# Optimization experiments

Hardware: AMD Instinct MI355X
Metric: run time of the kernel (lower is better)

## Reference

```python
import jax, jax.numpy as jnp
import jax.lax as lax
import numpy as np

PS = 5           # patch_w for rgb (arch_opt.rgb=True)
PAD = PS // 2    # 2
WS = 29          # search window
SRAD = WS // 2   # 14
K = 14           # neigh_pad: number of nearest neighbors kept


def setup_inputs() -> dict:
    key = jax.random.key(0)
    k1, k2 = jax.random.split(key)
    noisy = jax.random.uniform(k1, (1, 3, 256, 256), jnp.float32) * 255.0
    sigma = jnp.array([25.0], jnp.float32)
    w_gray = jnp.array([0.2989, 0.587, 0.114], jnp.float32)  # fixed rgb2gray conv weight
    return {"noisy": noisy, "sigma": sigma, "w_gray": w_gray}


def reference(noisy, sigma, w_gray):
    t, c, h, w = noisy.shape
    # rescale to [-1,1] and remove per-image mean (as in forward)
    x = (noisy / 255.0 - 0.5) / 0.5
    means = x.mean((-2, -1), keepdims=True)
    x = x - means

    # grayscale search image (rgb2gray 1x1 conv)
    g = jnp.einsum('tchw,c->thw', x, w_gray)
    padT = PAD + SRAD  # 16: patch halo + search radius
    Gp = jnp.pad(g, ((0, 0), (padT, padT), (padT, padT)), mode='reflect')

    # --- patch-SSD over all ws*ws window offsets (KNN search) ---
    offs = jnp.arange(WS * WS)
    dys, dxs = offs // WS, offs % WS  # 0..28 <-> true offset -14..14
    Hc, Wc = h + 2 * PAD, w + 2 * PAD

    def crop(dy, dx):  # shifted crop covering all query patch supports
        return lax.dynamic_slice(Gp, (0, dy, dx), (t, Hc, Wc))

    S = jax.vmap(crop)(dys, dxs)                                   # [O,t,Hc,Wc]
    Cc = lax.dynamic_slice(Gp, (0, SRAD, SRAD), (t, Hc, Wc))       # center crop
    diff2 = (Cc[None] - S) ** 2                                    # [O,t,Hc,Wc]
    O = WS * WS
    kern = jnp.ones((1, 1, PS, PS), jnp.float32)
    d = lax.conv_general_dilated(diff2.reshape(O * t, 1, Hc, Wc), kern,
                                 (1, 1), 'VALID',
                                 dimension_numbers=('NCHW', 'OIHW', 'NCHW'))
    dists = d.reshape(O, t, h, w).transpose(1, 2, 3, 0)            # [t,h,w,O]

    negd, idx = lax.top_k(-dists, K)                               # k nearest offsets
    dists_k = -negd                                                # [t,h,w,K]

    # --- gather neighbor color patches ---
    Xp = jnp.pad(x, ((0, 0), (0, 0), (padT, padT), (padT, padT)), mode='reflect')
    patches = lax.conv_general_dilated_patches(Xp, (PS, PS), (1, 1), 'VALID')
    D = c * PS * PS
    Hg, Wg = h + 2 * SRAD, w + 2 * SRAD   # patch-center grid incl. search halo
    pf = patches.reshape(t, D, Hg * Wg)
    dy, dx = idx // WS, idx % WS          # 0..28; grid row = i + dy
    ii = jnp.arange(h)[None, :, None, None]
    jj = jnp.arange(w)[None, None, :, None]
    flat = ((ii + dy) * Wg + (jj + dx)).reshape(t, -1)             # [t, h*w*K]
    gathered = jax.vmap(lambda p, f: jnp.take(p, f, axis=1))(pf, flat)
    gathered = gathered.reshape(t, D, h * w, K)                    # [t,D,Q,K]

    # --- distance-softmax weighted patch aggregation ---
    sig = sigma[0] / 127.5  # noise std in rescaled units
    wts = jax.nn.softmax(-dists_k.reshape(t, h * w, K) / (sig * sig * PS * PS + 1e-8), axis=-1)
    pden = jnp.einsum('tdqk,tqk->tdq', gathered, wts).reshape(t, c, PS, PS, h, w)

    # --- fold (overlap-add) denoised patches + count normalization ---
    out = jnp.zeros((t, c, Hc, Wc), jnp.float32)
    cnt = jnp.zeros((1, 1, Hc, Wc), jnp.float32)
    for p in range(PS):
        for q in range(PS):
            out = out.at[:, :, p:p + h, q:q + w].add(pden[:, :, p, q])
            cnt = cnt.at[:, :, p:p + h, q:q + w].add(1.0)
    deno = out[:, :, PAD:-PAD, PAD:-PAD] / cnt[:, :, PAD:-PAD, PAD:-PAD]

    deno = deno + means
    deno = 255.0 * (deno * 0.5 + 0.5)
    return deno
```

## Files before the change

### kernel.cpp

```cpp
#include <hip/hip_runtime.h>

#define EXT 40
#define SQ (EXT*EXT)

__device__ __forceinline__ unsigned um_min(unsigned a, unsigned b){ return a < b ? a : b; }
__device__ __forceinline__ unsigned um_max(unsigned a, unsigned b){ return a > b ? a : b; }

__device__ __forceinline__ void insert14(unsigned (&arr)[14], unsigned key){
  arr[0] = um_min(arr[0], key);
  #pragma unroll
  for (int s = 0; s < 13; ++s){
    unsigned a = arr[s], b = arr[s+1];
    arr[s]   = um_max(a, b);
    arr[s+1] = um_min(a, b);
  }
}

__global__ void k_prep(const float* __restrict__ noisy, float* __restrict__ Xp){
  int idx = blockIdx.x * 256 + threadIdx.x;
  if (idx >= 288*288) return;
  int P = idx / 288, Q = idx - P*288;
  int sy = P - 16; sy = sy < 0 ? -sy : sy; sy = sy > 255 ? 510 - sy : sy;
  int sx = Q - 16; sx = sx < 0 ? -sx : sx; sx = sx > 255 ? 510 - sx : sx;
  const float inv = 1.0f / 127.5f;
  int src = sy*256 + sx;
  #pragma unroll
  for (int c = 0; c < 3; ++c)
    Xp[c*82944 + idx] = noisy[c*65536 + src] * inv - 1.0f;
}

template<int R>
__device__ __forceinline__ void ssd_step(const float* rowbase, int dx, unsigned obase,
                                         float (&cp)[5][5], float (&win)[5][5],
                                         unsigned (&arr)[14]){
  constexpr int nc = (R + 4) % 5;
  #pragma unroll
  for (int u = 0; u < 5; ++u) win[u][nc] = rowbase[u*EXT + dx + 4];
  float s = 0.f;
  #pragma unroll
  for (int u = 0; u < 5; ++u){
    #pragma unroll
    for (int v = 0; v < 5; ++v){
      float d = cp[u][v] - win[u][(R + v) % 5];
      s = fmaf(d, d, s);
    }
  }
  insert14(arr, (__float_as_uint(s) & 0xFFFFFC00u) | (obase + (unsigned)dx));
}

__global__ __launch_bounds__(256, 4) void k_search(const float* __restrict__ Xp,
      const float* __restrict__ sigma, const float* __restrict__ wgray,
      float* __restrict__ accG){
  __shared__ float sXp[3*SQ];
  __shared__ float sG[SQ];
  __shared__ unsigned sCand[3*64*14];
  __shared__ float sWsum[64];
  __shared__ float sFold[12*12*3];

  const int tid = threadIdx.x;
  const int w = tid >> 6, l = tid & 63;
  const int ly = l >> 3, lx = l & 7;
  const int bi = blockIdx.y * 8, bj = blockIdx.x * 8;

  for (int t = tid; t < 3*SQ; t += 256){
    int c = t / SQ; int r2 = t - c*SQ; int rr = r2 / EXT; int cc = r2 - rr*EXT;
    sXp[t] = Xp[c*82944 + (bi+rr)*288 + (bj+cc)];
  }
  if (tid < 64) sWsum[tid] = 0.f;
  for (int t = tid; t < 432; t += 256) sFold[t] = 0.f;
  __syncthreads();
  const float w0 = wgray[0], w1 = wgray[1], w2 = wgray[2];
  for (int t = tid; t < SQ; t += 256)
    sG[t] = w0*sXp[t] + w1*sXp[SQ+t] + w2*sXp[2*SQ+t];
  __syncthreads();

  float cp[5][5];
  #pragma unroll
  for (int u = 0; u < 5; ++u)
    #pragma unroll
    for (int v = 0; v < 5; ++v)
      cp[u][v] = sG[(14 + ly + u)*EXT + 14 + lx + v];

  unsigned arr[14];
  #pragma unroll
  for (int k = 0; k < 14; ++k) arr[k] = 0xFFFFFFFFu;

  const int dy0 = (w == 0) ? 0 : 1 + 7*w;
  const int dy1 = dy0 + ((w == 0) ? 8 : 7);

  for (int dy = dy0; dy < dy1; ++dy){
    const float* rowbase = &sG[(dy + ly)*EXT + lx];
    float win[5][5];
    #pragma unroll
    for (int u = 0; u < 5; ++u)
      #pragma unroll
      for (int v = 0; v < 4; ++v)
        win[u][v] = rowbase[u*EXT + v];
    const unsigned obase = (unsigned)(dy * 29);

    for (int b = 0; b < 5; ++b){
      int dxb = b * 5;
      ssd_step<0>(rowbase, dxb+0, obase, cp, win, arr);
      ssd_step<1>(rowbase, dxb+1, obase, cp, win, arr);
      ssd_step<2>(rowbase, dxb+2, obase, cp, win, arr);
      ssd_step<3>(rowbase, dxb+3, obase, cp, win, arr);
      ssd_step<4>(rowbase, dxb+4, obase, cp, win, arr);
    }
    ssd_step<0>(rowbase, 25, obase, cp, win, arr);
    ssd_step<1>(rowbase, 26, obase, cp, win, arr);
    ssd_step<2>(rowbase, 27, obase, cp, win, arr);
    ssd_step<3>(rowbase, 28, obase, cp, win, arr);
  }

  if (w){
    #pragma unroll
    for (int k = 0; k < 14; ++k) sCand[((w-1)*64 + l)*14 + k] = arr[k];
  }
  __syncthreads();
  if (!w){
    for (int q = 0; q < 3; ++q)
      #pragma unroll
      for (int k = 0; k < 14; ++k)
        insert14(arr, sCand[(q*64 + l)*14 + k]);
    #pragma unroll
    for (int k = 0; k < 14; ++k) sCand[l*14 + k] = arr[k];
  }
  __syncthreads();

  float sg = sigma[0] * (1.0f / 127.5f);
  const float invT = 1.0f / (sg*sg*25.0f + 1e-8f);
  const float dmin = __uint_as_float(sCand[l*14 + 13] & 0xFFFFFC00u);

  float wgt[4]; int ndy[4], ndx[4];
  const int nk = (w < 2) ? 4 : 3;
  float Sp = 0.f;
  #pragma unroll
  for (int m = 0; m < 4; ++m){
    if (m < nk){
      unsigned kk = sCand[l*14 + (w + 4*m)];
      float d = __uint_as_float(kk & 0xFFFFFC00u);
      int o = (int)(kk & 0x3FFu);
      wgt[m] = expf(-(d - dmin) * invT);
      ndy[m] = o / 29; ndx[m] = o - ndy[m]*29;
      Sp += wgt[m];
    }
  }
  atomicAdd(&sWsum[l], Sp);
  __syncthreads();
  const float invS = 1.0f / sWsum[l];
  #pragma unroll
  for (int m = 0; m < 4; ++m) if (m < nk) wgt[m] *= invS;

  #pragma unroll
  for (int c = 0; c < 3; ++c){
    float acc[5][5];
    #pragma unroll
    for (int u = 0; u < 5; ++u)
      #pragma unroll
      for (int v = 0; v < 5; ++v) acc[u][v] = 0.f;
    #pragma unroll
    for (int m = 0; m < 4; ++m){
      if (m < nk){
        const float* pb = &sXp[c*SQ + (ly + ndy[m])*EXT + lx + ndx[m]];
        float g = wgt[m];
        #pragma unroll
        for (int u = 0; u < 5; ++u)
          #pragma unroll
          for (int v = 0; v < 5; ++v)
            acc[u][v] = fmaf(g, pb[u*EXT + v], acc[u][v]);
      }
    }
    #pragma unroll
    for (int u = 0; u < 5; ++u)
      #pragma unroll
      for (int v = 0; v < 5; ++v)
        atomicAdd(&sFold[((ly+u)*12 + (lx+v))*3 + c], acc[u][v]);
  }
  __syncthreads();
  for (int t = tid; t < 432; t += 256){
    int c = t % 3; int rc = t / 3; int rr = rc / 12; int cc = rc - rr*12;
    atomicAdd(&accG[c*67600 + (bi+rr)*260 + (bj+cc)], sFold[t]);
  }
}

__global__ void k_finish(const float* __restrict__ accG, float* __restrict__ out){
  int idx = blockIdx.x * 256 + threadIdx.x;
  if (idx >= 3*65536) return;
  int c = idx >> 16; int rem = idx & 65535; int y = rem >> 8; int x = rem & 255;
  int cy = min(4, y + 2) - max(0, y - 253) + 1;
  int cx = min(4, x + 2) - max(0, x - 253) + 1;
  float v = accG[c*67600 + (y+2)*260 + (x+2)] / (float)(cy * cx);
  out[idx] = 127.5f * v + 127.5f;
}

extern "C" void kernel_launch(void* const* d_in, const int* in_sizes, int n_in,
                              void* d_out, int out_size, void* d_ws, size_t ws_size,
                              hipStream_t stream) {
  const float* noisy = (const float*)d_in[0];
  const float* sigma = (const float*)d_in[1];
  const float* wgray = (const float*)d_in[2];
  float* out  = (float*)d_out;
  float* Xp   = (float*)d_ws;
  float* accG = Xp + 3*288*288;

  hipMemsetAsync(accG, 0, 3*260*260*sizeof(float), stream);
  k_prep<<<dim3(324), dim3(256), 0, stream>>>(noisy, Xp);
  k_search<<<dim3(32, 32), dim3(256), 0, stream>>>(Xp, sigma, wgray, accG);
  k_finish<<<dim3(768), dim3(256), 0, stream>>>(accG, out);
}
```

Before: 254.9 us.

## Expand SSD into norms minus cross term, use med3 top-k insert, fuse memset

```diff
diff --git a/kernel.cpp b/kernel.cpp
--- a/kernel.cpp
+++ b/kernel.cpp
@@ -5,19 +5,29 @@
 
 __device__ __forceinline__ unsigned um_min(unsigned a, unsigned b){ return a < b ? a : b; }
 __device__ __forceinline__ unsigned um_max(unsigned a, unsigned b){ return a > b ? a : b; }
-
-__device__ __forceinline__ void insert14(unsigned (&arr)[14], unsigned key){
-  arr[0] = um_min(arr[0], key);
-  #pragma unroll
-  for (int s = 0; s < 13; ++s){
-    unsigned a = arr[s], b = arr[s+1];
-    arr[s]   = um_max(a, b);
-    arr[s+1] = um_min(a, b);
-  }
-}
-
-__global__ void k_prep(const float* __restrict__ noisy, float* __restrict__ Xp){
+__device__ __forceinline__ unsigned med3u(unsigned a, unsigned b, unsigned c){
+  unsigned d;
+  asm("v_med3_u32 %0, %1, %2, %3" : "=v"(d) : "v"(a), "v"(b), "v"(c));
+  return d;
+}
+
+__device__ __forceinline__ void insert14(unsigned (&a)[14], unsigned key){
+  unsigned kp  = um_min(key, a[0]);
+  unsigned n0  = um_max(a[1], kp);
+  unsigned n13 = um_min(a[13], kp);
+  unsigned nn[12];
+  #pragma unroll
+  for (int i = 1; i <= 12; ++i) nn[i-1] = med3u(a[i], a[i+1], kp);
+  a[0] = n0;
+  #pragma unroll
+  for (int i = 1; i <= 12; ++i) a[i] = nn[i-1];
+  a[13] = n13;
+}
+
+__global__ void k_prep(const float* __restrict__ noisy, float* __restrict__ Xp,
+                       float* __restrict__ accG){
   int idx = blockIdx.x * 256 + threadIdx.x;
+  if (idx < 3*260*260) accG[idx] = 0.f;
   if (idx >= 288*288) return;
   int P = idx / 288, Q = idx - P*288;
   int sy = P - 16; sy = sy < 0 ? -sy : sy; sy = sy > 255 ? 510 - sy : sy;
@@ -29,23 +39,44 @@
     Xp[c*82944 + idx] = noisy[c*65536 + src] * inv - 1.0f;
 }
 
-template<int R>
-__device__ __forceinline__ void ssd_step(const float* rowbase, int dx, unsigned obase,
-                                         float (&cp)[5][5], float (&win)[5][5],
-                                         unsigned (&arr)[14]){
-  constexpr int nc = (R + 4) % 5;
-  #pragma unroll
-  for (int u = 0; u < 5; ++u) win[u][nc] = rowbase[u*EXT + dx + 4];
-  float s = 0.f;
-  #pragma unroll
-  for (int u = 0; u < 5; ++u){
-    #pragma unroll
-    for (int v = 0; v < 5; ++v){
-      float d = cp[u][v] - win[u][(R + v) % 5];
-      s = fmaf(d, d, s);
-    }
-  }
-  insert14(arr, (__float_as_uint(s) & 0xFFFFFC00u) | (obase + (unsigned)dx));
+template<int DX>
+__device__ __forceinline__ void ssd_step(const float* rowbase, unsigned obase,
+                                         const float (&cp)[5][5], float cpsq,
+                                         float (&win)[5][5], float (&ring)[5],
+                                         float& winsq, unsigned (&arr)[14]){
+  constexpr int nc = (DX + 4) % 5;
+  #pragma unroll
+  for (int u = 0; u < 5; ++u) win[u][nc] = rowbase[u*EXT + DX + 4];
+  float nssq = win[0][nc]*win[0][nc];
+  #pragma unroll
+  for (int u = 1; u < 5; ++u) nssq = fmaf(win[u][nc], win[u][nc], nssq);
+  winsq += (nssq - ring[nc]);
+  ring[nc] = nssq;
+  float c0=0.f, c1=0.f, c2=0.f, c3=0.f, c4=0.f;
+  #pragma unroll
+  for (int v = 0; v < 5; ++v){
+    constexpr int dummy = 0; (void)dummy;
+    c0 = fmaf(cp[0][v], win[0][(DX + v) % 5], c0);
+    c1 = fmaf(cp[1][v], win[1][(DX + v) % 5], c1);
+    c2 = fmaf(cp[2][v], win[2][(DX + v) % 5], c2);
+    c3 = fmaf(cp[3][v], win[3][(DX + v) % 5], c3);
+    c4 = fmaf(cp[4][v], win[4][(DX + v) % 5], c4);
+  }
+  float cross = ((c0 + c1) + (c2 + c3)) + c4;
+  float dist = fmaf(cross, -2.0f, cpsq + winsq);
+  dist = fmaxf(dist, 0.0f);
+  insert14(arr, (__float_as_uint(dist) & 0xFFFFFC00u) | (obase + (unsigned)DX));
+}
+
+template<int DX>
+__device__ __forceinline__ void row_steps(const float* rowbase, unsigned obase,
+                                          const float (&cp)[5][5], float cpsq,
+                                          float (&win)[5][5], float (&ring)[5],
+                                          float& winsq, unsigned (&arr)[14]){
+  if constexpr (DX < 29){
+    ssd_step<DX>(rowbase, obase, cp, cpsq, win, ring, winsq, arr);
+    row_steps<DX+1>(rowbase, obase, cp, cpsq, win, ring, winsq, arr);
+  }
 }
 
 __global__ __launch_bounds__(256, 4) void k_search(const float* __restrict__ Xp,
@@ -80,6 +111,14 @@
     #pragma unroll
     for (int v = 0; v < 5; ++v)
       cp[u][v] = sG[(14 + ly + u)*EXT + 14 + lx + v];
+  float cpsq = 0.f;
+  #pragma unroll
+  for (int v = 0; v < 5; ++v){
+    float cs = cp[0][v]*cp[0][v];
+    #pragma unroll
+    for (int u = 1; u < 5; ++u) cs = fmaf(cp[u][v], cp[u][v], cs);
+    cpsq += cs;
+  }
 
   unsigned arr[14];
   #pragma unroll
@@ -88,28 +127,22 @@
   const int dy0 = (w == 0) ? 0 : 1 + 7*w;
   const int dy1 = dy0 + ((w == 0) ? 8 : 7);
 
+  #pragma unroll 1
   for (int dy = dy0; dy < dy1; ++dy){
     const float* rowbase = &sG[(dy + ly)*EXT + lx];
-    float win[5][5];
-    #pragma unroll
-    for (int u = 0; u < 5; ++u)
-      #pragma unroll
-      for (int v = 0; v < 4; ++v)
-        win[u][v] = rowbase[u*EXT + v];
-    const unsigned obase = (unsigned)(dy * 29);
-
-    for (int b = 0; b < 5; ++b){
-      int dxb = b * 5;
-      ssd_step<0>(rowbase, dxb+0, obase, cp, win, arr);
-      ssd_step<1>(rowbase, dxb+1, obase, cp, win, arr);
-      ssd_step<2>(rowbase, dxb+2, obase, cp, win, arr);
-      ssd_step<3>(rowbase, dxb+3, obase, cp, win, arr);
-      ssd_step<4>(rowbase, dxb+4, obase, cp, win, arr);
+    float win[5][5], ring[5], winsq;
+    #pragma unroll
+    for (int v = 0; v < 4; ++v){
+      #pragma unroll
+      for (int u = 0; u < 5; ++u) win[u][v] = rowbase[u*EXT + v];
+      float cs = win[0][v]*win[0][v];
+      #pragma unroll
+      for (int u = 1; u < 5; ++u) cs = fmaf(win[u][v], win[u][v], cs);
+      ring[v] = cs;
     }
-    ssd_step<0>(rowbase, 25, obase, cp, win, arr);
-    ssd_step<1>(rowbase, 26, obase, cp, win, arr);
-    ssd_step<2>(rowbase, 27, obase, cp, win, arr);
-    ssd_step<3>(rowbase, 28, obase, cp, win, arr);
+    ring[4] = 0.f;
+    winsq = (ring[0] + ring[1]) + (ring[2] + ring[3]);
+    row_steps<0>(rowbase, (unsigned)(dy*29), cp, cpsq, win, ring, winsq, arr);
   }
 
   if (w){
@@ -203,8 +236,7 @@
   float* Xp   = (float*)d_ws;
   float* accG = Xp + 3*288*288;
 
-  hipMemsetAsync(accG, 0, 3*260*260*sizeof(float), stream);
-  k_prep<<<dim3(324), dim3(256), 0, stream>>>(noisy, Xp);
+  k_prep<<<dim3(793), dim3(256), 0, stream>>>(noisy, Xp, accG);
   k_search<<<dim3(32, 32), dim3(256), 0, stream>>>(Xp, sigma, wgray, accG);
   k_finish<<<dim3(768), dim3(256), 0, stream>>>(accG, out);
 }
```

After: 232.5 us. 8.8% less time.
